# Kernel tuning notes

Measured on AMD Instinct MI355X. Metric: run time of the kernel, lower is better.

## Reference

```python
import jax, jax.numpy as jnp
import numpy as np

D = 768
N_TASKS = 4


def setup_inputs() -> dict:
    key = jax.random.key(0)
    k1, k2, k3, k4, k5 = jax.random.split(key, 5)
    b, s, t = 8, 1024, 1024
    source_features = jax.random.normal(k1, (b, s, D), dtype=jnp.float32)
    target_features = jax.random.normal(k2, (b, t, D), dtype=jnp.float32)
    # learned params: nn.Linear(768,1) + Sigmoid, nn.Embedding(4,768), alpha
    W_cost = jax.random.normal(k3, (D, 1), dtype=jnp.float32) / np.sqrt(D)
    b_cost = jnp.zeros((1,), dtype=jnp.float32)
    task_emb = jax.random.normal(k4, (N_TASKS, D), dtype=jnp.float32)
    alpha = jnp.float32(0.05)
    return {
        "source_features": source_features,
        "target_features": target_features,
        "W_cost": W_cost,
        "b_cost": b_cost,
        "task_emb": task_emb,
        "alpha": alpha,
        "task_id": 2,
    }


def reference(source_features, target_features, W_cost, b_cost, task_emb, alpha, task_id):
    # metric='cosine': elementwise cos of the raw dot-product matrix (as in source)
    dots = jnp.einsum("bsd,btd->bst", source_features, target_features)
    cost = (1.0 - jnp.cos(dots)) / 2.0  # [b,s,t]

    # use_kernel_cost=True: gaussian kernel with h = 1 * std (unbiased, over last two dims)
    std = jnp.std(cost, axis=(-1, -2), keepdims=True, ddof=1)
    cost = jnp.exp(-((cost / std) ** 2) / 2.0)

    # train_cost_matrix=True: conditional MLP on (src + tgt + task_fea), Linear(768,1)+Sigmoid.
    # Linear is applied before the nonlinearity, so decompose to avoid the [b,s,t,768] tensor.
    s_proj = jnp.einsum("bsd,d->bs", source_features, W_cost[:, 0])  # [b,s]
    t_proj = jnp.einsum("btd,d->bt", target_features, W_cost[:, 0])  # [b,t]
    task_proj = jnp.dot(task_emb[task_id], W_cost[:, 0])  # scalar
    cond = jax.nn.sigmoid(
        s_proj[:, :, None] + t_proj[:, None, :] + task_proj + b_cost[0]
    )  # [b,s,t]

    cost = alpha * (cost + cond)
    return cost
```

## Files before the change

kernel.cpp:

```cpp
#include <hip/hip_runtime.h>
#include <hip/hip_bf16.h>
#include <math.h>

#define BATCHES 8
#define SEQ 1024
#define DDIM 768
#define NPANEL 8
#define NK64 12
#define CHUNK_B 16384
#define NK32 24
#define CHUNK_U 8192
#define QMAX 6.35f

typedef unsigned short u16;
typedef __attribute__((ext_vector_type(8))) short bf16x8;
typedef __attribute__((ext_vector_type(8))) unsigned short u16x8;
typedef __attribute__((ext_vector_type(4))) float f32x4;
typedef __attribute__((ext_vector_type(4))) int i32x4;

static __device__ __forceinline__ u16 f2bf(float x) {
    union { float f; unsigned u; } v; v.f = x;
    unsigned r = v.u + 0x7FFFu + ((v.u >> 16) & 1u);
    return (u16)(r >> 16);
}
static __device__ __forceinline__ float bf2f(u16 h) {
    union { float f; unsigned u; } v; v.u = ((unsigned)h) << 16; return v.f;
}

__device__ __forceinline__ void glds16(const void* g, void* l) {
    __builtin_amdgcn_global_load_lds(
        (const __attribute__((address_space(1))) void*)g,
        (__attribute__((address_space(3))) void*)l, 16, 0, 0);
}

__global__ __launch_bounds__(256) void prep_i8(
    const float* __restrict__ S, const float* __restrict__ T,
    const float* __restrict__ W, const float* __restrict__ bcost,
    const float* __restrict__ temb, const int* __restrict__ task_id,
    unsigned char* __restrict__ Sg, unsigned char* __restrict__ Tg,
    float* __restrict__ sproj, float* __restrict__ tproj,
    float* __restrict__ cterm)
{
    int t = threadIdx.x;
    int g = blockIdx.x * 256 + t;
    int r  = g & 15;
    int kg = (g >> 4) & 3;
    int m  = (g >> 6) & 7;
    int x  = g >> 9;
    int ks = x % NK64; x /= NK64;
    int p  = x & 7;
    int b  = (x >> 3) & 7;
    int tensor = x >> 6;

    int row_loc = p * 128 + m * 16 + r;
    int row_glb = b * SEQ + row_loc;
    int col = ks * 64 + kg * 16;

    const float* src = (tensor ? T : S) + (size_t)row_glb * DDIM + col;
    float4 f0 = *(const float4*)(src);
    float4 f1 = *(const float4*)(src + 4);
    float4 f2 = *(const float4*)(src + 8);
    float4 f3 = *(const float4*)(src + 12);
    float4 w0 = *(const float4*)(W + col);
    float4 w1 = *(const float4*)(W + col + 4);
    float4 w2 = *(const float4*)(W + col + 8);
    float4 w3 = *(const float4*)(W + col + 12);

    float xv[16] = {f0.x,f0.y,f0.z,f0.w, f1.x,f1.y,f1.z,f1.w,
                    f2.x,f2.y,f2.z,f2.w, f3.x,f3.y,f3.z,f3.w};
    float wv[16] = {w0.x,w0.y,w0.z,w0.w, w1.x,w1.y,w1.z,w1.w,
                    w2.x,w2.y,w2.z,w2.w, w3.x,w3.y,w3.z,w3.w};

    float pd = 0.f;
    #pragma unroll
    for (int e = 0; e < 16; ++e) pd = fmaf(xv[e], wv[e], pd);
    pd += __shfl_down(pd, 32);
    pd += __shfl_down(pd, 16);
    if ((t & 63) < 16)
        atomicAdd((tensor ? tproj : sproj) + row_glb, pd);

    const float s     = QMAX / 127.0f;
    const float inv_s = 127.0f / QMAX;
    const float inv_s2 = 252.0f / s;
    unsigned q1w[4] = {0,0,0,0}, q2w[4] = {0,0,0,0};
    #pragma unroll
    for (int e = 0; e < 16; ++e) {
        float v = xv[e];
        float q1f = rintf(v * inv_s);
        q1f = fminf(fmaxf(q1f, -127.f), 127.f);
        float rr = fmaf(-q1f, s, v);
        float q2f = rintf(rr * inv_s2);
        q2f = fminf(fmaxf(q2f, -126.f), 126.f);
        unsigned b1 = (unsigned)(unsigned char)(char)(int)q1f;
        unsigned b2 = (unsigned)(unsigned char)(char)(int)q2f;
        q1w[e >> 2] |= b1 << ((e & 3) * 8);
        q2w[e >> 2] |= b2 << ((e & 3) * 8);
    }
    unsigned char* dst = (tensor ? Tg : Sg)
        + (size_t)((b * NPANEL + p) * NK64 + ks) * CHUNK_B
        + (m * 1024 + kg * 256 + r * 16);
    *(uint4*)dst          = (uint4){q1w[0], q1w[1], q1w[2], q1w[3]};
    *(uint4*)(dst + 8192) = (uint4){q2w[0], q2w[1], q2w[2], q2w[3]};

    if (blockIdx.x == 0 && t < 64) {
        int tid = *task_id;
        float sacc = 0.f;
        #pragma unroll
        for (int d = t; d < DDIM; d += 64) sacc = fmaf(temb[tid * DDIM + d], W[d], sacc);
        #pragma unroll
        for (int o = 32; o; o >>= 1) sacc += __shfl_down(sacc, o);
        if (t == 0) *cterm = sacc + bcost[0];
    }
}

__global__ __launch_bounds__(256) void proj_kernel(
    const float* __restrict__ S, const float* __restrict__ T,
    const float* __restrict__ W, const float* __restrict__ bcost,
    const float* __restrict__ temb, const int* __restrict__ task_id,
    float* __restrict__ sproj, float* __restrict__ tproj,
    float* __restrict__ cterm)
{
    int gw   = (blockIdx.x * blockDim.x + threadIdx.x) >> 6;
    int lane = threadIdx.x & 63;

    if (gw < 2 * BATCHES * SEQ) {
        const float* rowp = (gw < BATCHES * SEQ)
            ? S + (size_t)gw * DDIM
            : T + (size_t)(gw - BATCHES * SEQ) * DDIM;
        float s = 0.f;
        #pragma unroll
        for (int d = lane; d < DDIM; d += 64) s = fmaf(rowp[d], W[d], s);
        #pragma unroll
        for (int o = 32; o; o >>= 1) s += __shfl_down(s, o);
        if (lane == 0) {
            if (gw < BATCHES * SEQ) sproj[gw] = s;
            else                    tproj[gw - BATCHES * SEQ] = s;
        }
    }
    if (blockIdx.x == gridDim.x - 1 && (threadIdx.x >> 6) == 0) {
        int tid = *task_id;
        float s = 0.f;
        #pragma unroll
        for (int d = lane; d < DDIM; d += 64) s = fmaf(temb[tid * DDIM + d], W[d], s);
        #pragma unroll
        for (int o = 32; o; o >>= 1) s += __shfl_down(s, o);
        if (lane == 0) *cterm = s + bcost[0];
    }
}

__global__ __launch_bounds__(256) void gemm_i8(
    const unsigned char* __restrict__ Sg, const unsigned char* __restrict__ Tg,
    float* __restrict__ out, double* __restrict__ batch_sums)
{
    __shared__ __align__(16) unsigned char lds[2][32768];
    __shared__ double red[8];

    const int t    = threadIdx.x;
    const int lane = t & 63;
    const int w    = t >> 6;
    const int wr   = w >> 1, wc = w & 1;

    int wg = (blockIdx.x & 7) * 64 + (blockIdx.x >> 3);
    const int b  = wg >> 6;
    const int by = (wg >> 3) & 7;
    const int bx = wg & 7;

    i32x4 acc_hh[4][4], acc_x[4][4];
    #pragma unroll
    for (int m = 0; m < 4; ++m)
        #pragma unroll
        for (int n = 0; n < 4; ++n) {
            acc_hh[m][n] = (i32x4){0,0,0,0};
            acc_x[m][n]  = (i32x4){0,0,0,0};
        }

    const unsigned char* Achunk = Sg + (size_t)((b * NPANEL + by) * NK64) * CHUNK_B;
    const unsigned char* Bchunk = Tg + (size_t)((b * NPANEL + bx) * NK64) * CHUNK_B;

    auto STAGE = [&](int ks, int buf) {
        const unsigned char* src = (w < 2 ? Achunk : Bchunk)
                                 + (size_t)ks * CHUNK_B + (w & 1) * 8192 + lane * 16;
        unsigned char* dst = &lds[buf][w * 8192];
        #pragma unroll
        for (int j = 0; j < 8; ++j)
            glds16(src + j * 1024, dst + j * 1024);
    };
    auto COMPUTE = [&](const unsigned char* L) {
        i32x4 a1[4], a2[4], b1[4], b2[4];
        #pragma unroll
        for (int m = 0; m < 4; ++m) {
            int sm = wr * 4 + m;
            a1[m] = *(const i32x4*)(L + sm * 1024 + lane * 16);
            a2[m] = *(const i32x4*)(L + 8192 + sm * 1024 + lane * 16);
        }
        #pragma unroll
        for (int n = 0; n < 4; ++n) {
            int sn = wc * 4 + n;
            b1[n] = *(const i32x4*)(L + 16384 + sn * 1024 + lane * 16);
            b2[n] = *(const i32x4*)(L + 24576 + sn * 1024 + lane * 16);
        }
        #pragma unroll
        for (int m = 0; m < 4; ++m)
            #pragma unroll
            for (int n = 0; n < 4; ++n) {
                acc_hh[m][n] = __builtin_amdgcn_mfma_i32_16x16x64_i8(a1[m], b1[n], acc_hh[m][n], 0, 0, 0);
                acc_x[m][n]  = __builtin_amdgcn_mfma_i32_16x16x64_i8(a1[m], b2[n], acc_x[m][n], 0, 0, 0);
                acc_x[m][n]  = __builtin_amdgcn_mfma_i32_16x16x64_i8(a2[m], b1[n], acc_x[m][n], 0, 0, 0);
            }
    };

    STAGE(0, 0);
    #pragma unroll 1
    for (int it = 0; it < NK64; ++it) {
        asm volatile("s_waitcnt vmcnt(0)" ::: "memory");
        __builtin_amdgcn_s_barrier();
        __builtin_amdgcn_sched_barrier(0);
        if (it + 1 < NK64) STAGE(it + 1, (it + 1) & 1);
        COMPUTE(&lds[it & 1][0]);
        asm volatile("s_waitcnt lgkmcnt(0)" ::: "memory");
    }

    const float S2  = (QMAX / 127.0f) * (QMAX / 127.0f);
    const float S2F = S2 / 252.0f;
    float lsum = 0.f, lsq = 0.f;
    float* outb = out + (size_t)b * SEQ * SEQ;
    const int rbase = by * 128 + wr * 64;
    const int cbase = bx * 128 + wc * 64;
    const int cr = lane >> 4;
    const int cc = lane & 15;
    #pragma unroll
    for (int m = 0; m < 4; ++m) {
        #pragma unroll
        for (int n = 0; n < 4; ++n) {
            int col = cbase + n * 16 + cc;
            #pragma unroll
            for (int j = 0; j < 4; ++j) {
                int row = rbase + m * 16 + cr * 4 + j;
                float d  = S2 * (float)acc_hh[m][n][j] + S2F * (float)acc_x[m][n][j];
                float c0 = 0.5f - 0.5f * __cosf(d);
                outb[(size_t)row * SEQ + col] = c0;
                lsum += c0;
                lsq  = fmaf(c0, c0, lsq);
            }
        }
    }

    double s = (double)lsum, q = (double)lsq;
    #pragma unroll
    for (int o = 32; o; o >>= 1) { s += __shfl_down(s, o); q += __shfl_down(q, o); }
    if (lane == 0) { red[w] = s; red[4 + w] = q; }
    __syncthreads();
    if (t == 0) {
        s = red[0] + red[1] + red[2] + red[3];
        q = red[4] + red[5] + red[6] + red[7];
        atomicAdd(&batch_sums[b * 2 + 0], s);
        atomicAdd(&batch_sums[b * 2 + 1], q);
    }
}

__global__ __launch_bounds__(256) void gemm_fused_bf16(
    const float* __restrict__ S, const float* __restrict__ T,
    float* __restrict__ out, double* __restrict__ batch_sums)
{
    __shared__ __align__(16) u16 lds[16384];
    __shared__ double red[8];

    const int t    = threadIdx.x;
    const int lane = t & 63;
    const int w    = t >> 6;
    const int wr   = w >> 1, wc = w & 1;

    int wg = (blockIdx.x & 7) * 64 + (blockIdx.x >> 3);
    const int b  = wg >> 6;
    const int by = (wg >> 3) & 7;
    const int bx = wg & 7;

    f32x4 acc[4][4];
    #pragma unroll
    for (int m = 0; m < 4; ++m)
        #pragma unroll
        for (int n = 0; n < 4; ++n) acc[m][n] = (f32x4){0.f, 0.f, 0.f, 0.f};

    const float* Sb = S + (size_t)b * SEQ * DDIM;
    const float* Tb = T + (size_t)b * SEQ * DDIM;
    const float* pa[2]; const float* pb[2];
    float4 ra[2][2], rb[2][2];
    #pragma unroll
    for (int i = 0; i < 2; ++i) {
        int g = t + i * 256;
        int m = g >> 6, kg = (g >> 4) & 3, r = g & 15;
        pa[i] = Sb + (size_t)(by * 128 + m * 16 + r) * DDIM + kg * 8;
        pb[i] = Tb + (size_t)(bx * 128 + m * 16 + r) * DDIM + kg * 8;
    }

    auto LOADREGS = [&](int ks) {
        #pragma unroll
        for (int i = 0; i < 2; ++i) {
            ra[i][0] = *(const float4*)(pa[i] + ks * 32);
            ra[i][1] = *(const float4*)(pa[i] + ks * 32 + 4);
            rb[i][0] = *(const float4*)(pb[i] + ks * 32);
            rb[i][1] = *(const float4*)(pb[i] + ks * 32 + 4);
        }
    };
    auto STAGE_FUSED = [&]() {
        #pragma unroll
        for (int i = 0; i < 2; ++i) {
            int g = t + i * 256;
            float xa[8] = {ra[i][0].x, ra[i][0].y, ra[i][0].z, ra[i][0].w,
                           ra[i][1].x, ra[i][1].y, ra[i][1].z, ra[i][1].w};
            float xb[8] = {rb[i][0].x, rb[i][0].y, rb[i][0].z, rb[i][0].w,
                           rb[i][1].x, rb[i][1].y, rb[i][1].z, rb[i][1].w};
            u16x8 ah, al, bh, bl;
            #pragma unroll
            for (int e = 0; e < 8; ++e) {
                u16 h = f2bf(xa[e]); ah[e] = h; al[e] = f2bf(xa[e] - bf2f(h));
                u16 g2 = f2bf(xb[e]); bh[e] = g2; bl[e] = f2bf(xb[e] - bf2f(g2));
            }
            *(u16x8*)&lds[(size_t)g * 8]         = ah;
            *(u16x8*)&lds[4096 + (size_t)g * 8]  = al;
            *(u16x8*)&lds[8192 + (size_t)g * 8]  = bh;
            *(u16x8*)&lds[12288 + (size_t)g * 8] = bl;
        }
    };
    auto COMPUTE = [&]() {
        const u16* L = &lds[0];
        bf16x8 ah[4], al[4], bh[4], bl[4];
        #pragma unroll
        for (int m = 0; m < 4; ++m) {
            int sm = wr * 4 + m;
            ah[m] = *(const bf16x8*)(L + sm * 512 + lane * 8);
            al[m] = *(const bf16x8*)(L + 4096 + sm * 512 + lane * 8);
        }
        #pragma unroll
        for (int n = 0; n < 4; ++n) {
            int sn = wc * 4 + n;
            bh[n] = *(const bf16x8*)(L + 8192 + sn * 512 + lane * 8);
            bl[n] = *(const bf16x8*)(L + 12288 + sn * 512 + lane * 8);
        }
        #pragma unroll
        for (int m = 0; m < 4; ++m)
            #pragma unroll
            for (int n = 0; n < 4; ++n) {
                acc[m][n] = __builtin_amdgcn_mfma_f32_16x16x32_bf16(ah[m], bh[n], acc[m][n], 0, 0, 0);
                acc[m][n] = __builtin_amdgcn_mfma_f32_16x16x32_bf16(ah[m], bl[n], acc[m][n], 0, 0, 0);
                acc[m][n] = __builtin_amdgcn_mfma_f32_16x16x32_bf16(al[m], bh[n], acc[m][n], 0, 0, 0);
            }
    };

    LOADREGS(0);
    for (int ks = 0; ks < NK32; ++ks) {
        STAGE_FUSED();
        __syncthreads();
        if (ks + 1 < NK32) LOADREGS(ks + 1);
        COMPUTE();
        __syncthreads();
    }

    float lsum = 0.f, lsq = 0.f;
    float* outb = out + (size_t)b * SEQ * SEQ;
    const int rbase = by * 128 + wr * 64;
    const int cbase = bx * 128 + wc * 64;
    const int cr = lane >> 4;
    const int cc = lane & 15;
    #pragma unroll
    for (int m = 0; m < 4; ++m) {
        #pragma unroll
        for (int n = 0; n < 4; ++n) {
            int col = cbase + n * 16 + cc;
            #pragma unroll
            for (int j = 0; j < 4; ++j) {
                int row = rbase + m * 16 + cr * 4 + j;
                float d  = acc[m][n][j];
                float c0 = 0.5f - 0.5f * __cosf(d);
                outb[(size_t)row * SEQ + col] = c0;
                lsum += c0;
                lsq  = fmaf(c0, c0, lsq);
            }
        }
    }

    double s = (double)lsum, q = (double)lsq;
    #pragma unroll
    for (int o = 32; o; o >>= 1) { s += __shfl_down(s, o); q += __shfl_down(q, o); }
    if (lane == 0) { red[w] = s; red[4 + w] = q; }
    __syncthreads();
    if (t == 0) {
        s = red[0] + red[1] + red[2] + red[3];
        q = red[4] + red[5] + red[6] + red[7];
        atomicAdd(&batch_sums[b * 2 + 0], s);
        atomicAdd(&batch_sums[b * 2 + 1], q);
    }
}

__global__ __launch_bounds__(256) void finalize_kernel(
    float* __restrict__ out, const double* __restrict__ batch_sums,
    const float* __restrict__ sproj, const float* __restrict__ tproj,
    const float* __restrict__ cterm_p, const float* __restrict__ alpha_p)
{
    const double n = (double)SEQ * (double)SEQ;
    size_t idx4 = (size_t)blockIdx.x * blockDim.x + threadIdx.x;
    size_t base = idx4 * 4;
    int batch = (int)(base >> 20);
    int rem   = (int)(base & ((SEQ * SEQ) - 1));
    int srow  = rem >> 10;
    int tcol  = rem & (SEQ - 1);

    double sum = batch_sums[batch * 2 + 0];
    double sq  = batch_sums[batch * 2 + 1];
    double var = (sq - sum * sum / n) / (n - 1.0);
    float inv_std = (float)(1.0 / sqrt(var));

    float alpha = *alpha_p;
    float ct    = *cterm_p;
    float sp    = sproj[batch * SEQ + srow];
    float4 tp   = *(const float4*)&tproj[batch * SEQ + tcol];
    float4 c    = *(float4*)&out[base];

    float4 r;
    { float x = c.x * inv_std; float g = __expf(-0.5f * x * x);
      float z = sp + tp.x + ct; float cd = 1.f / (1.f + __expf(-z)); r.x = alpha * (g + cd); }
    { float x = c.y * inv_std; float g = __expf(-0.5f * x * x);
      float z = sp + tp.y + ct; float cd = 1.f / (1.f + __expf(-z)); r.y = alpha * (g + cd); }
    { float x = c.z * inv_std; float g = __expf(-0.5f * x * x);
      float z = sp + tp.z + ct; float cd = 1.f / (1.f + __expf(-z)); r.z = alpha * (g + cd); }
    { float x = c.w * inv_std; float g = __expf(-0.5f * x * x);
      float z = sp + tp.w + ct; float cd = 1.f / (1.f + __expf(-z)); r.w = alpha * (g + cd); }
    *(float4*)&out[base] = r;
}

extern "C" void kernel_launch(void* const* d_in, const int* in_sizes, int n_in,
                              void* d_out, int out_size, void* d_ws, size_t ws_size,
                              hipStream_t stream) {
    const float* S      = (const float*)d_in[0];
    const float* T      = (const float*)d_in[1];
    const float* W      = (const float*)d_in[2];
    const float* bcost  = (const float*)d_in[3];
    const float* temb   = (const float*)d_in[4];
    const float* alpha  = (const float*)d_in[5];
    const int*   taskid = (const int*)d_in[6];
    float* out = (float*)d_out;

    double* batch_sums = (double*)d_ws;
    float*  sproj = (float*)((char*)d_ws + 128);
    float*  tproj = sproj + BATCHES * SEQ;
    float*  cterm = tproj + BATCHES * SEQ;

    const size_t ZERO_BYTES = 128 + sizeof(float) * (2 * BATCHES * SEQ + 1);
    const size_t SMALL = (size_t)1 << 20;
    const size_t CONV_B = (size_t)BATCHES * NPANEL * NK64 * CHUNK_B;
    const size_t NEEDED = SMALL + 2 * CONV_B;
    unsigned char* Sg = (unsigned char*)d_ws + SMALL;
    unsigned char* Tg = Sg + CONV_B;

    hipMemsetAsync(d_ws, 0, ZERO_BYTES, stream);

    if (ws_size >= NEEDED) {
        int nblk = (2 * BATCHES * NPANEL * NK64 * 512) / 256;
        prep_i8<<<nblk, 256, 0, stream>>>(S, T, W, bcost, temb, taskid,
                                          Sg, Tg, sproj, tproj, cterm);
        gemm_i8<<<512, 256, 0, stream>>>(Sg, Tg, out, batch_sums);
    } else {
        proj_kernel<<<4097, 256, 0, stream>>>(S, T, W, bcost, temb, taskid,
                                              sproj, tproj, cterm);
        gemm_fused_bf16<<<512, 256, 0, stream>>>(S, T, out, batch_sums);
    }

    int nblk2 = (BATCHES * SEQ * SEQ) / (256 * 4);
    finalize_kernel<<<nblk2, 256, 0, stream>>>(out, batch_sums, sproj, tproj,
                                               cterm, alpha);
}
```

Measured before the change: 74.59 us.

## Shrink int8 GEMM tile to 64x64 with single LDS buffer and more blocks

```diff
diff --git a/kernel.cpp b/kernel.cpp
--- a/kernel.cpp
+++ b/kernel.cpp
@@ -5,11 +5,10 @@
 #define BATCHES 8
 #define SEQ 1024
 #define DDIM 768
-#define NPANEL 8
+#define NPANEL 16
 #define NK64 12
-#define CHUNK_B 16384
+#define CHUNK_B 8192
 #define NK32 24
-#define CHUNK_U 8192
 #define QMAX 6.35f
 
 typedef unsigned short u16;
@@ -45,14 +44,15 @@
     int g = blockIdx.x * 256 + t;
     int r  = g & 15;
     int kg = (g >> 4) & 3;
-    int m  = (g >> 6) & 7;
-    int x  = g >> 9;
-    int ks = x % NK64; x /= NK64;
-    int p  = x & 7;
-    int b  = (x >> 3) & 7;
-    int tensor = x >> 6;
-
-    int row_loc = p * 128 + m * 16 + r;
+    int m  = (g >> 6) & 3;
+    int x  = g >> 8;
+    int ks = x % NK64;
+    int y  = x / NK64;
+    int p  = y & 15;
+    int b  = (y >> 4) & 7;
+    int tensor = y >> 7;
+
+    int row_loc = p * 64 + m * 16 + r;
     int row_glb = b * SEQ + row_loc;
     int col = ks * 64 + kg * 16;
 
@@ -74,10 +74,7 @@
     float pd = 0.f;
     #pragma unroll
     for (int e = 0; e < 16; ++e) pd = fmaf(xv[e], wv[e], pd);
-    pd += __shfl_down(pd, 32);
-    pd += __shfl_down(pd, 16);
-    if ((t & 63) < 16)
-        atomicAdd((tensor ? tproj : sproj) + row_glb, pd);
+    atomicAdd((tensor ? tproj : sproj) + row_glb, pd);
 
     const float s     = QMAX / 127.0f;
     const float inv_s = 127.0f / QMAX;
@@ -100,7 +97,7 @@
         + (size_t)((b * NPANEL + p) * NK64 + ks) * CHUNK_B
         + (m * 1024 + kg * 256 + r * 16);
     *(uint4*)dst          = (uint4){q1w[0], q1w[1], q1w[2], q1w[3]};
-    *(uint4*)(dst + 8192) = (uint4){q2w[0], q2w[1], q2w[2], q2w[3]};
+    *(uint4*)(dst + 4096) = (uint4){q2w[0], q2w[1], q2w[2], q2w[3]};
 
     if (blockIdx.x == 0 && t < 64) {
         int tid = *task_id;
@@ -148,11 +145,11 @@
     }
 }
 
-__global__ __launch_bounds__(256) void gemm_i8(
+__global__ __launch_bounds__(256, 4) void gemm_i8(
     const unsigned char* __restrict__ Sg, const unsigned char* __restrict__ Tg,
     float* __restrict__ out, double* __restrict__ batch_sums)
 {
-    __shared__ __align__(16) unsigned char lds[2][32768];
+    __shared__ __align__(16) unsigned char lds[16384];
     __shared__ double red[8];
 
     const int t    = threadIdx.x;
@@ -160,16 +157,16 @@
     const int w    = t >> 6;
     const int wr   = w >> 1, wc = w & 1;
 
-    int wg = (blockIdx.x & 7) * 64 + (blockIdx.x >> 3);
-    const int b  = wg >> 6;
-    const int by = (wg >> 3) & 7;
-    const int bx = wg & 7;
-
-    i32x4 acc_hh[4][4], acc_x[4][4];
-    #pragma unroll
-    for (int m = 0; m < 4; ++m)
-        #pragma unroll
-        for (int n = 0; n < 4; ++n) {
+    int wg = (blockIdx.x & 7) * 256 + (blockIdx.x >> 3);
+    const int b  = wg >> 8;
+    const int by = (wg >> 4) & 15;
+    const int bx = wg & 15;
+
+    i32x4 acc_hh[2][2], acc_x[2][2];
+    #pragma unroll
+    for (int m = 0; m < 2; ++m)
+        #pragma unroll
+        for (int n = 0; n < 2; ++n) {
             acc_hh[m][n] = (i32x4){0,0,0,0};
             acc_x[m][n]  = (i32x4){0,0,0,0};
         }
@@ -177,61 +174,59 @@
     const unsigned char* Achunk = Sg + (size_t)((b * NPANEL + by) * NK64) * CHUNK_B;
     const unsigned char* Bchunk = Tg + (size_t)((b * NPANEL + bx) * NK64) * CHUNK_B;
 
-    auto STAGE = [&](int ks, int buf) {
+    auto STAGE = [&](int ks) {
         const unsigned char* src = (w < 2 ? Achunk : Bchunk)
-                                 + (size_t)ks * CHUNK_B + (w & 1) * 8192 + lane * 16;
-        unsigned char* dst = &lds[buf][w * 8192];
-        #pragma unroll
-        for (int j = 0; j < 8; ++j)
+                                 + (size_t)ks * CHUNK_B + (w & 1) * 4096 + lane * 16;
+        unsigned char* dst = lds + w * 4096;
+        #pragma unroll
+        for (int j = 0; j < 4; ++j)
             glds16(src + j * 1024, dst + j * 1024);
     };
-    auto COMPUTE = [&](const unsigned char* L) {
-        i32x4 a1[4], a2[4], b1[4], b2[4];
-        #pragma unroll
-        for (int m = 0; m < 4; ++m) {
-            int sm = wr * 4 + m;
+    auto COMPUTE = [&]() {
+        const unsigned char* L = lds;
+        i32x4 a1[2], a2[2], b1[2], b2[2];
+        #pragma unroll
+        for (int m = 0; m < 2; ++m) {
+            int sm = wr * 2 + m;
             a1[m] = *(const i32x4*)(L + sm * 1024 + lane * 16);
-            a2[m] = *(const i32x4*)(L + 8192 + sm * 1024 + lane * 16);
-        }
-        #pragma unroll
-        for (int n = 0; n < 4; ++n) {
-            int sn = wc * 4 + n;
-            b1[n] = *(const i32x4*)(L + 16384 + sn * 1024 + lane * 16);
-            b2[n] = *(const i32x4*)(L + 24576 + sn * 1024 + lane * 16);
-        }
-        #pragma unroll
-        for (int m = 0; m < 4; ++m)
+            a2[m] = *(const i32x4*)(L + 4096 + sm * 1024 + lane * 16);
+        }
+        #pragma unroll
+        for (int n = 0; n < 2; ++n) {
+            int sn = wc * 2 + n;
+            b1[n] = *(const i32x4*)(L + 8192 + sn * 1024 + lane * 16);
+            b2[n] = *(const i32x4*)(L + 12288 + sn * 1024 + lane * 16);
+        }
+        #pragma unroll
+        for (int m = 0; m < 2; ++m)
             #pragma unroll
-            for (int n = 0; n < 4; ++n) {
+            for (int n = 0; n < 2; ++n) {
                 acc_hh[m][n] = __builtin_amdgcn_mfma_i32_16x16x64_i8(a1[m], b1[n], acc_hh[m][n], 0, 0, 0);
                 acc_x[m][n]  = __builtin_amdgcn_mfma_i32_16x16x64_i8(a1[m], b2[n], acc_x[m][n], 0, 0, 0);
                 acc_x[m][n]  = __builtin_amdgcn_mfma_i32_16x16x64_i8(a2[m], b1[n], acc_x[m][n], 0, 0, 0);
             }
     };
 
-    STAGE(0, 0);
     #pragma unroll 1
-    for (int it = 0; it < NK64; ++it) {
-        asm volatile("s_waitcnt vmcnt(0)" ::: "memory");
-        __builtin_amdgcn_s_barrier();
-        __builtin_amdgcn_sched_barrier(0);
-        if (it + 1 < NK64) STAGE(it + 1, (it + 1) & 1);
-        COMPUTE(&lds[it & 1][0]);
-        asm volatile("s_waitcnt lgkmcnt(0)" ::: "memory");
+    for (int ks = 0; ks < NK64; ++ks) {
+        STAGE(ks);
+        __syncthreads();
+        COMPUTE();
+        __syncthreads();
     }
 
     const float S2  = (QMAX / 127.0f) * (QMAX / 127.0f);
     const float S2F = S2 / 252.0f;
     float lsum = 0.f, lsq = 0.f;
     float* outb = out + (size_t)b * SEQ * SEQ;
-    const int rbase = by * 128 + wr * 64;
-    const int cbase = bx * 128 + wc * 64;
+    const int rbase = by * 64 + wr * 32;
+    const int cbase = bx * 64 + wc * 32;
     const int cr = lane >> 4;
     const int cc = lane & 15;
     #pragma unroll
-    for (int m = 0; m < 4; ++m) {
-        #pragma unroll
-        for (int n = 0; n < 4; ++n) {
+    for (int m = 0; m < 2; ++m) {
+        #pragma unroll
+        for (int n = 0; n < 2; ++n) {
             int col = cbase + n * 16 + cc;
             #pragma unroll
             for (int j = 0; j < 4; ++j) {
@@ -455,10 +450,10 @@
     hipMemsetAsync(d_ws, 0, ZERO_BYTES, stream);
 
     if (ws_size >= NEEDED) {
-        int nblk = (2 * BATCHES * NPANEL * NK64 * 512) / 256;
+        int nblk = (2 * BATCHES * NPANEL * NK64 * 256) / 256;
         prep_i8<<<nblk, 256, 0, stream>>>(S, T, W, bcost, temb, taskid,
                                           Sg, Tg, sproj, tproj, cterm);
-        gemm_i8<<<512, 256, 0, stream>>>(Sg, Tg, out, batch_sums);
+        gemm_i8<<<2048, 256, 0, stream>>>(Sg, Tg, out, batch_sums);
     } else {
         proj_kernel<<<4097, 256, 0, stream>>>(S, T, W, bcost, temb, taskid,
                                               sproj, tproj, cterm);
```

Measured after the change: 87.51 us. 1.17x slower.
